# Optimization experiments

Hardware: AMD Instinct MI355X
Metric: run time of the kernel (lower is better)

## Reference

```python
import jax, jax.numpy as jnp
import numpy as np

B, Cin, H, W = 8, 128, 64, 64
Cout, K, S, P = 128, 3, 1, 1
KK = K * K


def _conv(x, w, b=None):
    y = jax.lax.conv_general_dilated(
        x, w, window_strides=(S, S), padding=[(P, P), (P, P)],
        dimension_numbers=("NCHW", "OIHW", "NCHW"))
    if b is not None:
        y = y + b[None, :, None, None]
    return y


def setup_inputs() -> dict:
    key = jax.random.key(0)
    ks = jax.random.split(key, 6)
    x = jax.random.normal(ks[0], (B, Cin, H, W), jnp.float32)
    # offset/modulator convs are zero-init in the module; use small random
    # values so learned-offset sampling path is actually exercised.
    w_off = jax.random.normal(ks[1], (2 * KK, Cin, K, K), jnp.float32) * 0.01
    b_off = jax.random.normal(ks[2], (2 * KK,), jnp.float32) * 0.1
    w_mod = jax.random.normal(ks[3], (KK, Cin, K, K), jnp.float32) * 0.01
    b_mod = jax.random.normal(ks[4], (KK,), jnp.float32) * 0.1
    w_reg = jax.random.normal(ks[5], (Cout, Cin, K, K), jnp.float32) * (1.0 / np.sqrt(Cin * KK))
    return {"x": x, "w_off": w_off, "b_off": b_off,
            "w_mod": w_mod, "b_mod": b_mod, "w_reg": w_reg}


def _deform_conv2d(x, offset, mask, w_reg):
    # offset: [B, 2*KK, Hout, Wout] with (dy, dx) interleaved per tap (torchvision layout)
    Hout, Wout = offset.shape[2], offset.shape[3]
    off = offset.reshape(B, KK, 2, Hout, Wout)
    dy = off[:, :, 0].transpose(0, 2, 3, 1)  # [B,Hout,Wout,KK]
    dx = off[:, :, 1].transpose(0, 2, 3, 1)
    kh = (jnp.arange(KK) // K).astype(jnp.float32)
    kw = (jnp.arange(KK) % K).astype(jnp.float32)
    ho = jnp.arange(Hout, dtype=jnp.float32) * S - P
    wo = jnp.arange(Wout, dtype=jnp.float32) * S - P
    py = ho[None, :, None, None] + kh[None, None, None, :] + dy  # [B,Hout,Wout,KK]
    px = wo[None, None, :, None] + kw[None, None, None, :] + dx
    y0f = jnp.floor(py); x0f = jnp.floor(px)
    wy = (py - y0f)[..., None]; wx = (px - x0f)[..., None]
    y0 = y0f.astype(jnp.int32); x0 = x0f.astype(jnp.int32)
    x_bhwc = x.transpose(0, 2, 3, 1)  # [B,H,W,Cin]
    bidx = jnp.arange(B).reshape(B, 1, 1, 1)

    def gather(yi, xi):
        valid = ((yi >= 0) & (yi < H) & (xi >= 0) & (xi < W)).astype(x.dtype)
        v = x_bhwc[bidx, jnp.clip(yi, 0, H - 1), jnp.clip(xi, 0, W - 1)]
        return v * valid[..., None]  # [B,Hout,Wout,KK,Cin], zero outside

    v00 = gather(y0, x0)
    v01 = gather(y0, x0 + 1)
    v10 = gather(y0 + 1, x0)
    v11 = gather(y0 + 1, x0 + 1)
    val = (v00 * (1 - wy) * (1 - wx) + v01 * (1 - wy) * wx
           + v10 * wy * (1 - wx) + v11 * wy * wx)
    # modulated deformable conv v2: mask [B,KK,Hout,Wout]
    val = val * mask.transpose(0, 2, 3, 1)[..., None]
    # weighted accumulation over taps and input channels -> NCHW output
    return jnp.einsum("bhwkc,ock->bohw", val, w_reg.reshape(Cout, Cin, KK))


def reference(x, w_off, b_off, w_mod, b_mod, w_reg):
    offset = _conv(x, w_off, b_off)
    mask = 2.0 * jax.nn.sigmoid(_conv(x, w_mod, b_mod))
    return _deform_conv2d(x, offset, mask, w_reg)
```

## Files before the change

kernel.cpp:

```cpp
#include <hip/hip_runtime.h>
#include <hip/hip_bf16.h>
#include <math.h>

#define H 64
#define W 64
#define CIN 128
#define COUT 128
#define BATCH 8
#define NPIX (H*W)
#define PXT 32
#define AP  136

typedef __attribute__((ext_vector_type(8))) short bf16x8;
typedef __attribute__((ext_vector_type(4))) float f32x4;

static __device__ inline short f2bf(float f) {
  union { float f; unsigned u; } v; v.f = f;
  unsigned r = v.u + 0x7FFF + ((v.u >> 16) & 1);
  return (short)(r >> 16);
}
static __device__ inline float bf_lo(unsigned u) {
  union { unsigned u; float f; } v; v.u = u << 16; return v.f;
}
static __device__ inline float bf_hi(unsigned u) {
  union { unsigned u; float f; } v; v.u = u & 0xffff0000u; return v.f;
}

__global__ __launch_bounds__(256) void k_prep(const float* __restrict__ x,
    short* __restrict__ xbh,
    const float* __restrict__ w_off, const float* __restrict__ w_mod,
    short* __restrict__ wOMs, const float* __restrict__ w_reg,
    short* __restrict__ wAs) {
  __shared__ float tile[32][65];
  int blk = blockIdx.x;
  int t = threadIdx.x;
  if (blk < 2048) {
    int cg = blk & 3, y = (blk >> 2) & 63, b = blk >> 8;
#pragma unroll
    for (int j = 0; j < 8; ++j) {
      int idx = t + j * 256;
      int ci = idx >> 6, xi = idx & 63;
      tile[ci][xi] = x[(((b * CIN + cg * 32 + ci) * H + y) * W) + xi];
    }
    __syncthreads();
#pragma unroll
    for (int j = 0; j < 8; ++j) {
      int idx = t + j * 256;
      int xi = idx >> 5, ci = idx & 31;
      xbh[((b * H + y) * W + xi) * CIN + cg * 32 + ci] = f2bf(tile[ci][xi]);
    }
  } else if (blk < 2048 + 144) {
    int e = (blk - 2048) * 256 + t;
    int tap = e >> 12, oc = (e >> 7) & 31, c = e & 127;
    float v = 0.f;
    if (oc < 18)      v = w_off[(oc * 128 + c) * 9 + tap];
    else if (oc < 27) v = w_mod[((oc - 18) * 128 + c) * 9 + tap];
    int kb = c >> 5, quad = (c >> 3) & 3, j = c & 7;
    int g = oc >> 4, l16 = oc & 15;
    int o = ((tap * 4 + kb) * 2 + g) * 512 + (quad * 16 + l16) * 8 + j;
    wOMs[o] = f2bf(v);
  } else {
    int e = (blk - 2192) * 256 + t;
    int tap = e >> 14, oc = (e >> 7) & 127, c = e & 127;
    int kb = c >> 5, quad = (c >> 3) & 3, j = c & 7;
    int g = oc >> 4, l16 = oc & 15;
    int o = ((tap * 4 + kb) * 8 + g) * 512 + (quad * 16 + l16) * 8 + j;
    wAs[o] = f2bf(w_reg[(oc * 128 + c) * 9 + tap]);
  }
}

__global__ __launch_bounds__(512) void k_deform(const short* __restrict__ xbh,
    const short* __restrict__ wOMs, const float* __restrict__ b_off,
    const float* __restrict__ b_mod, const short* __restrict__ wAs,
    float* __restrict__ out) {
  __shared__ float red[8 * 1024];
  __shared__ __align__(16) short vs[PXT * AP];
  __shared__ __align__(16) float pw[PXT * 9 * 4];
  __shared__ __align__(16) int   pa[PXT * 9 * 4];

  int blk = blockIdx.x;
  int b = blk & 7, tile = blk >> 3;
  int pix0 = tile * PXT;
  int t = threadIdx.x;
  int lane = t & 63;
  int wv = t >> 6;
  int l16 = lane & 15, quad = lane >> 4;

  const short* xbB = xbh + (size_t)b * NPIX * CIN;

  {
    f32x4 acc_o[2][2] = {};
    for (int tap = wv; tap < 9; tap += 8) {
      const short* wt = wOMs + tap * 4096;
      int dy = tap / 3 - 1, dx = tap % 3 - 1;
      int lin[2], val[2];
#pragma unroll
      for (int nt = 0; nt < 2; ++nt) {
        int gp = pix0 + nt * 16 + l16;
        int y = (gp >> 6) + dy, x = (gp & 63) + dx;
        int ok = ((unsigned)y < H) && ((unsigned)x < W);
        val[nt] = ok;
        lin[nt] = ok ? ((y << 6) + x) : 0;
      }
#pragma unroll
      for (int kb = 0; kb < 4; ++kb) {
        bf16x8 a0 = *(const bf16x8*)&wt[(kb * 2 + 0) * 512 + lane * 8];
        bf16x8 a1 = *(const bf16x8*)&wt[(kb * 2 + 1) * 512 + lane * 8];
#pragma unroll
        for (int nt = 0; nt < 2; ++nt) {
          bf16x8 bv = *(const bf16x8*)&xbB[(size_t)lin[nt] * CIN + kb * 32 + quad * 8];
          if (!val[nt]) bv = (bf16x8){};
          acc_o[0][nt] = __builtin_amdgcn_mfma_f32_16x16x32_bf16(a0, bv, acc_o[0][nt], 0, 0, 0);
          acc_o[1][nt] = __builtin_amdgcn_mfma_f32_16x16x32_bf16(a1, bv, acc_o[1][nt], 0, 0, 0);
        }
      }
    }
#pragma unroll
    for (int mt = 0; mt < 2; ++mt)
#pragma unroll
      for (int nt = 0; nt < 2; ++nt)
#pragma unroll
        for (int r = 0; r < 4; ++r) {
          int oc = mt * 16 + quad * 4 + r;
          int px = nt * 16 + l16;
          red[wv * 1024 + oc * 32 + px] = acc_o[mt][nt][r];
        }
  }
  __syncthreads();

  for (int i = t; i < PXT * 9; i += 512) {
    int tap = i % 9, p = i / 9;
    float dyv = b_off[2 * tap], dxv = b_off[2 * tap + 1], z = b_mod[tap];
#pragma unroll
    for (int w = 0; w < 8; ++w) {
      dyv += red[w * 1024 + (2 * tap) * 32 + p];
      dxv += red[w * 1024 + (2 * tap + 1) * 32 + p];
      z   += red[w * 1024 + (18 + tap) * 32 + p];
    }
    float m = 2.f / (1.f + expf(-z));
    int gp = pix0 + p;
    float py = (float)((gp >> 6) - 1 + tap / 3) + dyv;
    float pxx = (float)((gp & 63) - 1 + tap % 3) + dxv;
    float yf = floorf(py), xf = floorf(pxx);
    float wy = py - yf, wx = pxx - xf;
    int y0 = (int)yf, x0 = (int)xf;
    int y1 = y0 + 1, x1 = x0 + 1;
    float vy0 = ((unsigned)y0 < H) ? 1.f : 0.f;
    float vy1 = ((unsigned)y1 < H) ? 1.f : 0.f;
    float vx0 = ((unsigned)x0 < W) ? 1.f : 0.f;
    float vx1 = ((unsigned)x1 < W) ? 1.f : 0.f;
    int y0c = min(max(y0, 0), H - 1), y1c = min(max(y1, 0), H - 1);
    int x0c = min(max(x0, 0), W - 1), x1c = min(max(x1, 0), W - 1);
    *(float4*)&pw[i * 4] = make_float4((1.f - wy) * (1.f - wx) * m * vy0 * vx0,
                                       (1.f - wy) * wx * m * vy0 * vx1,
                                       wy * (1.f - wx) * m * vy1 * vx0,
                                       wy * wx * m * vy1 * vx1);
    *(int4*)&pa[i * 4] = make_int4(((y0c << 6) + x0c) << 7,
                                   ((y0c << 6) + x1c) << 7,
                                   ((y1c << 6) + x0c) << 7,
                                   ((y1c << 6) + x1c) << 7);
  }

  int ms = wv & 3, nh = wv >> 2;
  int cq = t & 31, pxsub = (t >> 5) & 1, grp = t >> 6;
  int c0 = cq * 4;

  f32x4 acc[2] = {};

  for (int tap = 0; tap < 9; ++tap) {
    __syncthreads();

    const short* wtap = wAs + tap * 16384;
    bf16x8 af0[4], af1[4];
#pragma unroll
    for (int kb = 0; kb < 4; ++kb) {
      af0[kb] = *(const bf16x8*)&wtap[(kb * 8 + ms * 2) * 512 + lane * 8];
      af1[kb] = *(const bf16x8*)&wtap[(kb * 8 + ms * 2 + 1) * 512 + lane * 8];
    }

#pragma unroll
    for (int i = 0; i < 2; ++i) {
      int p = grp * 4 + i * 2 + pxsub;
      int idx = (p * 9 + tap) * 4;
      float4 wq = *(const float4*)&pw[idx];
      int4 aa = *(const int4*)&pa[idx];
      uint2 u00 = *(const uint2*)&xbB[aa.x + c0];
      uint2 u01 = *(const uint2*)&xbB[aa.y + c0];
      uint2 u10 = *(const uint2*)&xbB[aa.z + c0];
      uint2 u11 = *(const uint2*)&xbB[aa.w + c0];
      float s0 = wq.x * bf_lo(u00.x), s1 = wq.x * bf_hi(u00.x);
      float s2 = wq.x * bf_lo(u00.y), s3 = wq.x * bf_hi(u00.y);
      s0 = fmaf(wq.y, bf_lo(u01.x), s0); s1 = fmaf(wq.y, bf_hi(u01.x), s1);
      s2 = fmaf(wq.y, bf_lo(u01.y), s2); s3 = fmaf(wq.y, bf_hi(u01.y), s3);
      s0 = fmaf(wq.z, bf_lo(u10.x), s0); s1 = fmaf(wq.z, bf_hi(u10.x), s1);
      s2 = fmaf(wq.z, bf_lo(u10.y), s2); s3 = fmaf(wq.z, bf_hi(u10.y), s3);
      s0 = fmaf(wq.w, bf_lo(u11.x), s0); s1 = fmaf(wq.w, bf_hi(u11.x), s1);
      s2 = fmaf(wq.w, bf_lo(u11.y), s2); s3 = fmaf(wq.w, bf_hi(u11.y), s3);
      __hip_bfloat162 h2a = __float22bfloat162_rn(make_float2(s0, s1));
      __hip_bfloat162 h2b = __float22bfloat162_rn(make_float2(s2, s3));
      uint2 packed;
      packed.x = *(unsigned*)&h2a;
      packed.y = *(unsigned*)&h2b;
      *(uint2*)&vs[p * AP + c0] = packed;
    }
    __syncthreads();

#pragma unroll
    for (int kb = 0; kb < 4; ++kb) {
      int kcol = kb * 32 + quad * 8;
      bf16x8 b0 = *(const bf16x8*)&vs[(nh * 16 + l16) * AP + kcol];
      acc[0] = __builtin_amdgcn_mfma_f32_16x16x32_bf16(af0[kb], b0, acc[0], 0, 0, 0);
      acc[1] = __builtin_amdgcn_mfma_f32_16x16x32_bf16(af1[kb], b0, acc[1], 0, 0, 0);
    }
  }

  int oc_base = ms * 32;
#pragma unroll
  for (int mt = 0; mt < 2; ++mt)
#pragma unroll
    for (int r = 0; r < 4; ++r) {
      int oc = oc_base + mt * 16 + quad * 4 + r;
      int px = nh * 16 + l16;
      out[(size_t)(b * COUT + oc) * NPIX + pix0 + px] = acc[mt][r];
    }
}

extern "C" void kernel_launch(void* const* d_in, const int* in_sizes, int n_in,
                              void* d_out, int out_size, void* d_ws, size_t ws_size,
                              hipStream_t stream) {
  const float* x     = (const float*)d_in[0];
  const float* w_off = (const float*)d_in[1];
  const float* b_off = (const float*)d_in[2];
  const float* w_mod = (const float*)d_in[3];
  const float* b_mod = (const float*)d_in[4];
  const float* w_reg = (const float*)d_in[5];

  short* xbh  = (short*)d_ws;
  short* wAs  = xbh + 4194304;
  short* wOMs = wAs + 147456;
  float* out  = (float*)d_out;

  k_prep<<<dim3(2768), 256, 0, stream>>>(x, xbh, w_off, w_mod, wOMs,
                                         w_reg, wAs);
  k_deform<<<dim3(NPIX / PXT * BATCH), 512, 0, stream>>>(
      xbh, wOMs, b_off, b_mod, wAs, out);
}
```

Measured before the change: 131.2 us.

## Alias reduction and sample buffers in LDS, double-buffer taps, widen gather

Result: faster. 117.4 us (-10.5%).

```diff
diff --git a/kernel.cpp b/kernel.cpp
--- a/kernel.cpp
+++ b/kernel.cpp
@@ -10,6 +10,8 @@
 #define NPIX (H*W)
 #define PXT 32
 #define AP  136
+#define RP  36
+#define VSZ (PXT*AP)
 
 typedef __attribute__((ext_vector_type(8))) short bf16x8;
 typedef __attribute__((ext_vector_type(4))) float f32x4;
@@ -69,14 +71,15 @@
   }
 }
 
-__global__ __launch_bounds__(512) void k_deform(const short* __restrict__ xbh,
+__global__ __launch_bounds__(512, 8) void k_deform(const short* __restrict__ xbh,
     const short* __restrict__ wOMs, const float* __restrict__ b_off,
     const float* __restrict__ b_mod, const short* __restrict__ wAs,
     float* __restrict__ out) {
-  __shared__ float red[8 * 1024];
-  __shared__ __align__(16) short vs[PXT * AP];
+  __shared__ __align__(16) char smem_u[31104];
   __shared__ __align__(16) float pw[PXT * 9 * 4];
   __shared__ __align__(16) int   pa[PXT * 9 * 4];
+  float* red = (float*)smem_u;
+  short* vs  = (short*)smem_u;
 
   int blk = blockIdx.x;
   int b = blk & 7, tile = blk >> 3;
@@ -122,8 +125,10 @@
 #pragma unroll
         for (int r = 0; r < 4; ++r) {
           int oc = mt * 16 + quad * 4 + r;
-          int px = nt * 16 + l16;
-          red[wv * 1024 + oc * 32 + px] = acc_o[mt][nt][r];
+          if (oc < 27) {
+            int px = nt * 16 + l16;
+            red[wv * (27 * RP) + oc * RP + px] = acc_o[mt][nt][r];
+          }
         }
   }
   __syncthreads();
@@ -133,9 +138,10 @@
     float dyv = b_off[2 * tap], dxv = b_off[2 * tap + 1], z = b_mod[tap];
 #pragma unroll
     for (int w = 0; w < 8; ++w) {
-      dyv += red[w * 1024 + (2 * tap) * 32 + p];
-      dxv += red[w * 1024 + (2 * tap + 1) * 32 + p];
-      z   += red[w * 1024 + (18 + tap) * 32 + p];
+      const float* rw = red + w * (27 * RP);
+      dyv += rw[(2 * tap) * RP + p];
+      dxv += rw[(2 * tap + 1) * RP + p];
+      z   += rw[(18 + tap) * RP + p];
     }
     float m = 2.f / (1.f + expf(-z));
     int gp = pix0 + p;
@@ -160,15 +166,50 @@
                                    ((y1c << 6) + x0c) << 7,
                                    ((y1c << 6) + x1c) << 7);
   }
+  __syncthreads();
 
   int ms = wv & 3, nh = wv >> 2;
-  int cq = t & 31, pxsub = (t >> 5) & 1, grp = t >> 6;
-  int c0 = cq * 4;
+  int cq = t & 15, ps = t >> 4;
+  int c0 = cq * 8;
 
   f32x4 acc[2] = {};
 
   for (int tap = 0; tap < 9; ++tap) {
-    __syncthreads();
+    short* vbuf = vs + (tap & 1) * VSZ;
+
+    {
+      int idx = (ps * 9 + tap) * 4;
+      float4 wq = *(const float4*)&pw[idx];
+      int4 aa = *(const int4*)&pa[idx];
+      uint4 u00 = *(const uint4*)&xbB[aa.x + c0];
+      uint4 u01 = *(const uint4*)&xbB[aa.y + c0];
+      uint4 u10 = *(const uint4*)&xbB[aa.z + c0];
+      uint4 u11 = *(const uint4*)&xbB[aa.w + c0];
+      float s0 = wq.x * bf_lo(u00.x), s1 = wq.x * bf_hi(u00.x);
+      float s2 = wq.x * bf_lo(u00.y), s3 = wq.x * bf_hi(u00.y);
+      float s4 = wq.x * bf_lo(u00.z), s5 = wq.x * bf_hi(u00.z);
+      float s6 = wq.x * bf_lo(u00.w), s7 = wq.x * bf_hi(u00.w);
+      s0 = fmaf(wq.y, bf_lo(u01.x), s0); s1 = fmaf(wq.y, bf_hi(u01.x), s1);
+      s2 = fmaf(wq.y, bf_lo(u01.y), s2); s3 = fmaf(wq.y, bf_hi(u01.y), s3);
+      s4 = fmaf(wq.y, bf_lo(u01.z), s4); s5 = fmaf(wq.y, bf_hi(u01.z), s5);
+      s6 = fmaf(wq.y, bf_lo(u01.w), s6); s7 = fmaf(wq.y, bf_hi(u01.w), s7);
+      s0 = fmaf(wq.z, bf_lo(u10.x), s0); s1 = fmaf(wq.z, bf_hi(u10.x), s1);
+      s2 = fmaf(wq.z, bf_lo(u10.y), s2); s3 = fmaf(wq.z, bf_hi(u10.y), s3);
+      s4 = fmaf(wq.z, bf_lo(u10.z), s4); s5 = fmaf(wq.z, bf_hi(u10.z), s5);
+      s6 = fmaf(wq.z, bf_lo(u10.w), s6); s7 = fmaf(wq.z, bf_hi(u10.w), s7);
+      s0 = fmaf(wq.w, bf_lo(u11.x), s0); s1 = fmaf(wq.w, bf_hi(u11.x), s1);
+      s2 = fmaf(wq.w, bf_lo(u11.y), s2); s3 = fmaf(wq.w, bf_hi(u11.y), s3);
+      s4 = fmaf(wq.w, bf_lo(u11.z), s4); s5 = fmaf(wq.w, bf_hi(u11.z), s5);
+      s6 = fmaf(wq.w, bf_lo(u11.w), s6); s7 = fmaf(wq.w, bf_hi(u11.w), s7);
+      __hip_bfloat162 h0 = __float22bfloat162_rn(make_float2(s0, s1));
+      __hip_bfloat162 h1 = __float22bfloat162_rn(make_float2(s2, s3));
+      __hip_bfloat162 h2 = __float22bfloat162_rn(make_float2(s4, s5));
+      __hip_bfloat162 h3 = __float22bfloat162_rn(make_float2(s6, s7));
+      uint4 packed;
+      packed.x = *(unsigned*)&h0; packed.y = *(unsigned*)&h1;
+      packed.z = *(unsigned*)&h2; packed.w = *(unsigned*)&h3;
+      *(uint4*)&vbuf[ps * AP + c0] = packed;
+    }
 
     const short* wtap = wAs + tap * 16384;
     bf16x8 af0[4], af1[4];
@@ -177,38 +218,12 @@
       af0[kb] = *(const bf16x8*)&wtap[(kb * 8 + ms * 2) * 512 + lane * 8];
       af1[kb] = *(const bf16x8*)&wtap[(kb * 8 + ms * 2 + 1) * 512 + lane * 8];
     }
-
-#pragma unroll
-    for (int i = 0; i < 2; ++i) {
-      int p = grp * 4 + i * 2 + pxsub;
-      int idx = (p * 9 + tap) * 4;
-      float4 wq = *(const float4*)&pw[idx];
-      int4 aa = *(const int4*)&pa[idx];
-      uint2 u00 = *(const uint2*)&xbB[aa.x + c0];
-      uint2 u01 = *(const uint2*)&xbB[aa.y + c0];
-      uint2 u10 = *(const uint2*)&xbB[aa.z + c0];
-      uint2 u11 = *(const uint2*)&xbB[aa.w + c0];
-      float s0 = wq.x * bf_lo(u00.x), s1 = wq.x * bf_hi(u00.x);
-      float s2 = wq.x * bf_lo(u00.y), s3 = wq.x * bf_hi(u00.y);
-      s0 = fmaf(wq.y, bf_lo(u01.x), s0); s1 = fmaf(wq.y, bf_hi(u01.x), s1);
-      s2 = fmaf(wq.y, bf_lo(u01.y), s2); s3 = fmaf(wq.y, bf_hi(u01.y), s3);
-      s0 = fmaf(wq.z, bf_lo(u10.x), s0); s1 = fmaf(wq.z, bf_hi(u10.x), s1);
-      s2 = fmaf(wq.z, bf_lo(u10.y), s2); s3 = fmaf(wq.z, bf_hi(u10.y), s3);
-      s0 = fmaf(wq.w, bf_lo(u11.x), s0); s1 = fmaf(wq.w, bf_hi(u11.x), s1);
-      s2 = fmaf(wq.w, bf_lo(u11.y), s2); s3 = fmaf(wq.w, bf_hi(u11.y), s3);
-      __hip_bfloat162 h2a = __float22bfloat162_rn(make_float2(s0, s1));
-      __hip_bfloat162 h2b = __float22bfloat162_rn(make_float2(s2, s3));
-      uint2 packed;
-      packed.x = *(unsigned*)&h2a;
-      packed.y = *(unsigned*)&h2b;
-      *(uint2*)&vs[p * AP + c0] = packed;
-    }
     __syncthreads();
 
 #pragma unroll
     for (int kb = 0; kb < 4; ++kb) {
       int kcol = kb * 32 + quad * 8;
-      bf16x8 b0 = *(const bf16x8*)&vs[(nh * 16 + l16) * AP + kcol];
+      bf16x8 b0 = *(const bf16x8*)&vbuf[(nh * 16 + l16) * AP + kcol];
       acc[0] = __builtin_amdgcn_mfma_f32_16x16x32_bf16(af0[kb], b0, acc[0], 0, 0, 0);
       acc[1] = __builtin_amdgcn_mfma_f32_16x16x32_bf16(af1[kb], b0, acc[1], 0, 0, 0);
     }
```
